# Performance work log

Hardware: AMD Instinct MI355X
Metric: run time of the kernel (lower is better)

## Reference

```python
import jax, jax.numpy as jnp
import numpy as np

N = 4_000_000
POINT_DIM = 2
FEAT_OUT = 64
NUM_SEGMENTS = 4096


def setup_inputs() -> dict:
    key = jax.random.key(0)
    k1, k2, k3, k4 = jax.random.split(key, 4)
    x = jax.random.normal(k1, (N, POINT_DIM), dtype=jnp.float32)
    segment_ids = jnp.sort(jax.random.randint(k2, (N,), 0, NUM_SEGMENTS, dtype=jnp.int64 if jax.config.jax_enable_x64 else jnp.int32))
    W = jax.random.normal(k3, (POINT_DIM, FEAT_OUT), dtype=jnp.float32) / np.sqrt(POINT_DIM)
    b = jax.random.normal(k4, (FEAT_OUT,), dtype=jnp.float32)
    return {"x": x, "segment_ids": segment_ids, "W": W, "b": b, "num_segments": NUM_SEGMENTS}


def reference(x, segment_ids, W, b, num_segments):
    # phi: per-point linear projection, [N, point_dim] -> [N, feat_out]
    h = x @ W + b
    # 'add' aggregation over each set == segment sum (ids are sorted per-set)
    out = jax.ops.segment_sum(h, segment_ids, num_segments=num_segments,
                              indices_are_sorted=True)
    return out  # [num_segments, feat_out]
```

## Files before the change

### kernel.cpp

```cpp
#include <hip/hip_runtime.h>
#include <stdint.h>

#define NSEG 4096


__global__ __launch_bounds__(256) void seg_reduce(
    const float4* __restrict__ x4,
    const int4*   __restrict__ ids4,
    float* __restrict__ acc,
    int nchunk, int nchunk_w)
{
    const int lane = threadIdx.x & 63;
    const int stride = gridDim.x * blockDim.x;

    for (int chunk = blockIdx.x * blockDim.x + threadIdx.x; chunk < nchunk_w; chunk += stride) {
        const bool valid = chunk < nchunk;

        int4 idA, idB;
        float4 xA, xB, xC, xD;
        if (valid) {
            idA = ids4[2 * chunk];
            idB = ids4[2 * chunk + 1];
            xA = x4[4 * chunk + 0];
            xB = x4[4 * chunk + 1];
            xC = x4[4 * chunk + 2];
            xD = x4[4 * chunk + 3];
        } else {
            idA = make_int4(-1, -1, -1, -1);
            idB = idA;
            xA = make_float4(0.f, 0.f, 0.f, 0.f);
            xB = xC = xD = xA;
        }

        int   cur = idA.x;
        float s0 = xA.x, s1 = xA.y, cnt = valid ? 1.f : 0.f;

        #define PROC(SEG, X0, X1)                                          \
            if ((SEG) != cur) {                                            \
                if (cur >= 0) {                                            \
                    atomicAdd(&acc[4 * cur + 0], s0);                      \
                    atomicAdd(&acc[4 * cur + 1], s1);                      \
                    atomicAdd(&acc[4 * cur + 2], cnt);                     \
                }                                                          \
                cur = (SEG); s0 = (X0); s1 = (X1); cnt = 1.f;              \
            } else {                                                       \
                s0 += (X0); s1 += (X1); cnt += valid ? 1.f : 0.f;          \
            }

        PROC(idA.y, xA.z, xA.w)
        PROC(idA.z, xB.x, xB.y)
        PROC(idA.w, xB.z, xB.w)
        PROC(idB.x, xC.x, xC.y)
        PROC(idB.y, xC.z, xC.w)
        PROC(idB.z, xD.x, xD.y)
        PROC(idB.w, xD.z, xD.w)
        #undef PROC

        int prev = __shfl_up(cur, 1);
        bool head = (lane == 0) || (prev != cur);
        uint64_t heads = __ballot(head);
        uint64_t below = heads & (~0ull >> (63 - lane));
        int run_start = 63 - __builtin_clzll(below);

        #pragma unroll
        for (int d = 1; d < 64; d <<= 1) {
            float t0 = __shfl_up(s0, d);
            float t1 = __shfl_up(s1, d);
            float tc = __shfl_up(cnt, d);
            if (lane - d >= run_start) { s0 += t0; s1 += t1; cnt += tc; }
        }

        bool tail = (lane == 63) || ((heads >> (lane + 1)) & 1ull);
        if (tail && cur >= 0) {
            atomicAdd(&acc[4 * cur + 0], s0);
            atomicAdd(&acc[4 * cur + 1], s1);
            atomicAdd(&acc[4 * cur + 2], cnt);
        }
    }
}

__global__ __launch_bounds__(256) void epilogue(
    const float* __restrict__ acc,
    const float* __restrict__ W,
    const float* __restrict__ b,
    float* __restrict__ out)
{
    int idx = blockIdx.x * blockDim.x + threadIdx.x;
    int s = idx >> 6;
    int f = idx & 63;
    out[idx] = acc[4 * s] * W[f] + acc[4 * s + 1] * W[64 + f] + acc[4 * s + 2] * b[f];
}

extern "C" void kernel_launch(void* const* d_in, const int* in_sizes, int n_in,
                              void* d_out, int out_size, void* d_ws, size_t ws_size,
                              hipStream_t stream) {
    const float4* x4   = (const float4*)d_in[0];
    const int4*   ids4 = (const int4*)d_in[1];
    const float*  W    = (const float*)d_in[2];
    const float*  b    = (const float*)d_in[3];
    float* out = (float*)d_out;

    const int n = in_sizes[1];
    const int nchunk = n / 8;
    const int nchunk_w = (nchunk + 63) & ~63;

    float* acc = (float*)d_ws;

    hipMemsetAsync(d_ws, 0, 4 * NSEG * sizeof(float), stream);

    seg_reduce<<<2048, 256, 0, stream>>>(x4, ids4, acc, nchunk, nchunk_w);
    epilogue<<<(NSEG * 64) / 256, 256, 0, stream>>>(acc, W, b, out);
}
```

Measured before the change: 92.48 us.

## Fuse projection epilogue into segment reduce with per-feature atomics to output

Removes the separate epilogue kernel and the 4-float accumulator workspace. Each thread's completed segment partial sums are projected through W and b and atomically added straight into the 64-wide output rows. Wave-cooperative shuffles spread the 64 features across lanes for the first-closed and tail segments, and a serial 64-atomic loop handles any further segments. This saves a kernel launch but multiplies atomic traffic by roughly 64/3 per flushed partial, and it memsets the larger output buffer.

```diff
diff --git a/kernel.cpp b/kernel.cpp
--- a/kernel.cpp
+++ b/kernel.cpp
@@ -2,19 +2,26 @@
 #include <stdint.h>
 
 #define NSEG 4096
+#define FOUT 64
 
-
-__global__ __launch_bounds__(256) void seg_reduce(
+__global__ __launch_bounds__(256) void seg_reduce_fused(
     const float4* __restrict__ x4,
     const int4*   __restrict__ ids4,
-    float* __restrict__ acc,
+    const float*  __restrict__ W,
+    const float*  __restrict__ b,
+    float* __restrict__ out,
     int nchunk, int nchunk_w)
 {
     const int lane = threadIdx.x & 63;
     const int stride = gridDim.x * blockDim.x;
 
+    const float w0 = W[lane];
+    const float w1 = W[FOUT + lane];
+    const float bv = b[lane];
+
     for (int chunk = blockIdx.x * blockDim.x + threadIdx.x; chunk < nchunk_w; chunk += stride) {
         const bool valid = chunk < nchunk;
+        const float vinc = valid ? 1.f : 0.f;
 
         int4 idA, idB;
         float4 xA, xB, xC, xD;
@@ -33,18 +40,27 @@
         }
 
         int   cur = idA.x;
-        float s0 = xA.x, s1 = xA.y, cnt = valid ? 1.f : 0.f;
+        float s0 = xA.x, s1 = xA.y, cnt = vinc;
 
-        #define PROC(SEG, X0, X1)                                          \
-            if ((SEG) != cur) {                                            \
-                if (cur >= 0) {                                            \
-                    atomicAdd(&acc[4 * cur + 0], s0);                      \
-                    atomicAdd(&acc[4 * cur + 1], s1);                      \
-                    atomicAdd(&acc[4 * cur + 2], cnt);                     \
-                }                                                          \
-                cur = (SEG); s0 = (X0); s1 = (X1); cnt = 1.f;              \
-            } else {                                                       \
-                s0 += (X0); s1 += (X1); cnt += valid ? 1.f : 0.f;          \
+        int   pseg = -1;
+        float p0 = 0.f, p1 = 0.f, pc = 0.f;
+
+        #define PROC(SEG, X0, X1)                                              \
+            if ((SEG) != cur) {                                                \
+                if (cur >= 0) {                                                \
+                    if (pseg < 0) {                                            \
+                        pseg = cur; p0 = s0; p1 = s1; pc = cnt;                \
+                    } else {                                                   \
+                               \
+                              \
+                        for (int f = 0; f < FOUT; ++f)                         \
+                            atomicAdd(&out[(size_t)cur * FOUT + f],            \
+                                      s0 * W[f] + s1 * W[FOUT + f] + cnt * b[f]); \
+                    }                                                          \
+                }                                                              \
+                cur = (SEG); s0 = (X0); s1 = (X1); cnt = 1.f;                  \
+            } else {                                                           \
+                s0 += (X0); s1 += (X1); cnt += vinc;                           \
             }
 
         PROC(idA.y, xA.z, xA.w)
@@ -71,24 +87,29 @@
         }
 
         bool tail = (lane == 63) || ((heads >> (lane + 1)) & 1ull);
-        if (tail && cur >= 0) {
-            atomicAdd(&acc[4 * cur + 0], s0);
-            atomicAdd(&acc[4 * cur + 1], s1);
-            atomicAdd(&acc[4 * cur + 2], cnt);
+
+        uint64_t pm = __ballot(pseg >= 0);
+        while (pm) {
+            int t = __ffsll((unsigned long long)pm) - 1;
+            pm &= pm - 1;
+            int   fs = __shfl(pseg, t);
+            float f0 = __shfl(p0, t);
+            float f1 = __shfl(p1, t);
+            float fc = __shfl(pc, t);
+            atomicAdd(&out[(size_t)fs * FOUT + lane], f0 * w0 + f1 * w1 + fc * bv);
+        }
+
+        uint64_t tm = __ballot(tail && cur >= 0);
+        while (tm) {
+            int t = __ffsll((unsigned long long)tm) - 1;
+            tm &= tm - 1;
+            int   fs = __shfl(cur, t);
+            float f0 = __shfl(s0, t);
+            float f1 = __shfl(s1, t);
+            float fc = __shfl(cnt, t);
+            atomicAdd(&out[(size_t)fs * FOUT + lane], f0 * w0 + f1 * w1 + fc * bv);
         }
     }
-}
-
-__global__ __launch_bounds__(256) void epilogue(
-    const float* __restrict__ acc,
-    const float* __restrict__ W,
-    const float* __restrict__ b,
-    float* __restrict__ out)
-{
-    int idx = blockIdx.x * blockDim.x + threadIdx.x;
-    int s = idx >> 6;
-    int f = idx & 63;
-    out[idx] = acc[4 * s] * W[f] + acc[4 * s + 1] * W[64 + f] + acc[4 * s + 2] * b[f];
 }
 
 extern "C" void kernel_launch(void* const* d_in, const int* in_sizes, int n_in,
@@ -104,10 +125,7 @@
     const int nchunk = n / 8;
     const int nchunk_w = (nchunk + 63) & ~63;
 
-    float* acc = (float*)d_ws;
+    hipMemsetAsync(d_out, 0, NSEG * FOUT * sizeof(float), stream);
 
-    hipMemsetAsync(d_ws, 0, 4 * NSEG * sizeof(float), stream);
-
-    seg_reduce<<<2048, 256, 0, stream>>>(x4, ids4, acc, nchunk, nchunk_w);
-    epilogue<<<(NSEG * 64) / 256, 256, 0, stream>>>(acc, W, b, out);
+    seg_reduce_fused<<<2048, 256, 0, stream>>>(x4, ids4, W, b, out, nchunk, nchunk_w);
 }
```

Result: faster. 90.58 us (-2.1%).
